# Performance work log

Measured on AMD Instinct MI355X. Metric: run time of the kernel, lower is better.

Reference implementation:

```python
import jax, jax.numpy as jnp
import numpy as np

H, KVH, D, THETA = 32, 8, 128, 10000.0

def _rotate_half(x):
    x1, x2 = x[..., : D // 2], x[..., D // 2 :]
    return jnp.concatenate((-x2, x1), axis=-1)

def _rope_tables(seq_len, dtype):
    inv_freq = 1.0 / (THETA ** (jnp.arange(0, D, 2, dtype=jnp.float32) / D))
    t = jnp.arange(seq_len, dtype=jnp.float32)
    freqs = jnp.outer(t, inv_freq)                # [S, D/2]
    emb = jnp.concatenate((freqs, freqs), axis=-1)  # [S, D]
    return jnp.cos(emb).astype(dtype), jnp.sin(emb).astype(dtype)

def setup_inputs() -> dict:
    key = jax.random.key(0)
    ks = jax.random.split(key, 6)
    B, S, HID = 1, 2048, H * D
    hidden_states = jax.random.normal(ks[0], (B, S, HID), jnp.float32)
    # additive causal mask (bsz, 1, q_len, kv_seq_len)
    causal = jnp.tril(jnp.ones((S, S), dtype=bool))
    attention_mask = jnp.where(causal, 0.0, jnp.finfo(jnp.float32).min)[None, None].astype(jnp.float32)
    position_ids = jnp.arange(S, dtype=jnp.int32)[None, :]
    sc = 0.02
    Wq = jax.random.normal(ks[1], (H * D, HID), jnp.float32) * sc
    Wk = jax.random.normal(ks[2], (KVH * D, HID), jnp.float32) * sc
    Wv = jax.random.normal(ks[3], (KVH * D, HID), jnp.float32) * sc
    Wo = jax.random.normal(ks[4], (HID, H * D), jnp.float32) * sc
    return dict(hidden_states=hidden_states, attention_mask=attention_mask,
                position_ids=position_ids, Wq=Wq, Wk=Wk, Wv=Wv, Wo=Wo)

def reference(hidden_states, attention_mask, position_ids, Wq, Wk, Wv, Wo):
    B, S, HID = hidden_states.shape
    n_rep = H // KVH
    # projections -> [B, h, S, D]
    q = (hidden_states @ Wq.T).reshape(B, S, H, D).transpose(0, 2, 1, 3)
    k = (hidden_states @ Wk.T).reshape(B, S, KVH, D).transpose(0, 2, 1, 3)
    v = (hidden_states @ Wv.T).reshape(B, S, KVH, D).transpose(0, 2, 1, 3)
    # RoPE (cos/sin gathered by position_ids, broadcast over heads)
    cos_t, sin_t = _rope_tables(S, hidden_states.dtype)
    cos = cos_t[position_ids][:, None]            # [B, 1, S, D]
    sin = sin_t[position_ids][:, None]
    q = q * cos + _rotate_half(q) * sin
    k = k * cos + _rotate_half(k) * sin
    # GQA: repeat_kv == repeat_interleave over head dim
    k = jnp.repeat(k, n_rep, axis=1)
    v = jnp.repeat(v, n_rep, axis=1)
    scores = jnp.einsum('bhqd,bhkd->bhqk', q, k) / jnp.sqrt(jnp.float32(D)).astype(q.dtype)
    scores = scores + attention_mask
    probs = jax.nn.softmax(scores.astype(jnp.float32), axis=-1).astype(q.dtype)
    attn = jnp.einsum('bhqk,bhkd->bhqd', probs, v)  # [B, H, S, D]
    attn = attn.transpose(0, 2, 1, 3).reshape(B, S, H * D)
    return attn @ Wo.T
```

## Files before the change

kernel.cpp:

```cpp
#include <hip/hip_runtime.h>
#include <hip/hip_bf16.h>

typedef __bf16 bf16;
typedef __attribute__((ext_vector_type(8))) __bf16 bf16x8;
typedef __attribute__((ext_vector_type(2))) __bf16 bf16x2;
typedef __attribute__((ext_vector_type(4))) float f32x4;

#define GLL16(g, l)                                                        \
  __builtin_amdgcn_global_load_lds(                                        \
      (const __attribute__((address_space(1))) unsigned int*)(g),          \
      (__attribute__((address_space(3))) unsigned int*)(l), 16, 0, 0)

__global__ void cvt_f32_bf16(const float* __restrict__ in,
                             bf16* __restrict__ out, long n) {
  long i = ((long)blockIdx.x * blockDim.x + threadIdx.x) * 8;
  if (i >= n) return;
  f32x4 a = *reinterpret_cast<const f32x4*>(in + i);
  f32x4 b = *reinterpret_cast<const f32x4*>(in + i + 4);
  bf16x8 o;
  o[0] = (bf16)a[0]; o[1] = (bf16)a[1]; o[2] = (bf16)a[2]; o[3] = (bf16)a[3];
  o[4] = (bf16)b[0]; o[5] = (bf16)b[1]; o[6] = (bf16)b[2]; o[7] = (bf16)b[3];
  *reinterpret_cast<bf16x8*>(out + i) = o;
}

template <typename CT>
__device__ __forceinline__ void gemm_body(const bf16* __restrict__ A,
                                          const float* __restrict__ B,
                                          CT* __restrict__ C,
                                          int bm, int bn, int N, int K) {
  __shared__ __align__(16) bf16 As[2][4096];
  __shared__ __align__(16) bf16 Bs[2][4096];
  const int t = threadIdx.x;
  const int lane = t & 63;
  const int w = t >> 6;
  const int wr = w >> 2, wc = w & 3;
  const int fr = lane & 15, fg = lane >> 4;

  const int sr = t >> 2;
  const int sc = (t & 3) * 8;
  const bf16* gA = A + (long)(bm + sr) * K + sc;
  const float* gB = B + (long)(bn + sr) * K + sc;

  f32x4 acc[4][2];
#pragma unroll
  for (int m = 0; m < 4; m++)
#pragma unroll
    for (int n = 0; n < 2; n++) acc[m][n] = (f32x4){0.f, 0.f, 0.f, 0.f};

  auto stageB = [&](int buf, int k0) {
    f32x4 b0 = *reinterpret_cast<const f32x4*>(gB + k0);
    f32x4 b1 = *reinterpret_cast<const f32x4*>(gB + k0 + 4);
    bf16x8 bb;
    bb[0] = (bf16)b0[0]; bb[1] = (bf16)b0[1];
    bb[2] = (bf16)b0[2]; bb[3] = (bf16)b0[3];
    bb[4] = (bf16)b1[0]; bb[5] = (bf16)b1[1];
    bb[6] = (bf16)b1[2]; bb[7] = (bf16)b1[3];
    *reinterpret_cast<bf16x8*>(&Bs[buf][t * 8]) = bb;
  };

  {
    GLL16(gA, &As[0][t * 8]);
    stageB(0, 0);
  }
  int cur = 0;
  for (int k0 = 0; k0 < K; k0 += 32) {
    __syncthreads();
    if (k0 + 32 < K) {
      GLL16(gA + k0 + 32, &As[cur ^ 1][t * 8]);
      stageB(cur ^ 1, k0 + 32);
    }
    bf16x8 af[4], bfr[2];
#pragma unroll
    for (int m = 0; m < 4; m++)
      af[m] = *reinterpret_cast<const bf16x8*>(
          &As[cur][(wr * 64 + m * 16 + fr) * 32 + fg * 8]);
#pragma unroll
    for (int n = 0; n < 2; n++)
      bfr[n] = *reinterpret_cast<const bf16x8*>(
          &Bs[cur][(wc * 32 + n * 16 + fr) * 32 + fg * 8]);
#pragma unroll
    for (int m = 0; m < 4; m++)
#pragma unroll
      for (int n = 0; n < 2; n++)
        acc[m][n] =
            __builtin_amdgcn_mfma_f32_16x16x32_bf16(af[m], bfr[n], acc[m][n], 0, 0, 0);
    cur ^= 1;
  }
#pragma unroll
  for (int m = 0; m < 4; m++) {
#pragma unroll
    for (int n = 0; n < 2; n++) {
      const int row0 = bm + wr * 64 + m * 16 + fg * 4;
      const int col = bn + wc * 32 + n * 16 + fr;
#pragma unroll
      for (int j = 0; j < 4; j++)
        C[(long)(row0 + j) * N + col] = (CT)acc[m][n][j];
    }
  }
}

template <typename CT>
__global__ __launch_bounds__(512)
void gemm_bt(const bf16* __restrict__ A, const float* __restrict__ B,
             CT* __restrict__ C, int M, int N, int K) {
  gemm_body<CT>(A, B, C, blockIdx.y * 128, blockIdx.x * 128, N, K);
}

__global__ __launch_bounds__(512)
void gemm_qkv(const bf16* __restrict__ A, const float* __restrict__ Wq,
              const float* __restrict__ Wk, const float* __restrict__ Wv,
              bf16* __restrict__ qo, bf16* __restrict__ ko,
              bf16* __restrict__ vo) {
  const int nb = blockIdx.x;
  const float* B; bf16* C; int bn, N;
  if (nb < 32)      { B = Wq; C = qo; bn = nb * 128;        N = 4096; }
  else if (nb < 40) { B = Wk; C = ko; bn = (nb - 32) * 128; N = 1024; }
  else              { B = Wv; C = vo; bn = (nb - 40) * 128; N = 1024; }
  gemm_body<bf16>(A, B, C, blockIdx.y * 128, bn, N, 4096);
}

__global__ void rope_kernel(bf16* __restrict__ q, bf16* __restrict__ k,
                            const int* __restrict__ pos_ids) {
  int idx = blockIdx.x * blockDim.x + threadIdx.x;
  int s = idx / 2560;
  int rem = idx % 2560;
  int hh = rem >> 6;
  int dp = rem & 63;
  float p = (float)pos_ids[s];
  float freq = p * exp2f(-(float)dp * 0.20762050593046025f);
  float cs, sn;
  sincosf(freq, &sn, &cs);
  bf16* base = (hh < 32) ? (q + (long)s * 4096 + hh * 128)
                         : (k + (long)s * 1024 + (hh - 32) * 128);
  float x1 = (float)base[dp], x2 = (float)base[dp + 64];
  base[dp] = (bf16)(x1 * cs - x2 * sn);
  base[dp + 64] = (bf16)(x2 * cs + x1 * sn);
}

__global__ __launch_bounds__(256, 2)
void attn_fwd(const bf16* __restrict__ qg, const bf16* __restrict__ kg,
              const bf16* __restrict__ vg, bf16* __restrict__ og) {
  const int h = blockIdx.y;
  const int kvh = h >> 2;
  __shared__ __align__(16) bf16 Ks[64 * 128];
  __shared__ __align__(16) bf16 Vt[128 * 64];
  __shared__ __align__(16) bf16 Pm[4][16 * 64];
  const int t = threadIdx.x, lane = t & 63, w = t >> 6;
  const int fr = lane & 15, fg = lane >> 4;
  const float scale = 0.08838834764831845f;

  const int krow = t >> 2, kcol = (t & 3) * 32;
  const int vr = (t & 31) * 2, vd0 = (t >> 5) * 8;
  const bf16* gK = kg + kvh * 128;
  const bf16* gV = vg + kvh * 128;

#pragma unroll 1
  for (int half = 0; half < 2; half++) {
    const int qt = half == 0 ? (int)blockIdx.x : 31 - (int)blockIdx.x;
    const int q0 = qt * 64;
    const int wqmax = q0 + w * 16 + 15;
    const int qrow = q0 + w * 16 + fr;
    const int nt = qt + 1;

    bf16x8 aq[4];
#pragma unroll
    for (int c = 0; c < 4; c++)
      aq[c] = *reinterpret_cast<const bf16x8*>(
          &qg[(long)qrow * 4096 + h * 128 + c * 32 + fg * 8]);

    f32x4 oacc[8];
#pragma unroll
    for (int n = 0; n < 8; n++) oacc[n] = (f32x4){0.f, 0.f, 0.f, 0.f};
    float mrow[4], lrow[4];
#pragma unroll
    for (int j = 0; j < 4; j++) { mrow[j] = -INFINITY; lrow[j] = 0.f; }

    bf16x8 kst[4], vst[4];
    {
      const bf16* gk = gK + (long)krow * 1024 + kcol;
#pragma unroll
      for (int i = 0; i < 4; i++)
        kst[i] = *reinterpret_cast<const bf16x8*>(gk + 8 * i);
      const bf16* gv = gV + (long)vr * 1024 + vd0;
      vst[0] = *reinterpret_cast<const bf16x8*>(gv);
      vst[1] = *reinterpret_cast<const bf16x8*>(gv + 64);
      vst[2] = *reinterpret_cast<const bf16x8*>(gv + 1024);
      vst[3] = *reinterpret_cast<const bf16x8*>(gv + 1024 + 64);
    }

    for (int tt = 0; tt < nt; ++tt) {
      const int kv0 = tt * 64;
#pragma unroll
      for (int i = 0; i < 4; i++)
        *reinterpret_cast<bf16x8*>(
            &Ks[krow * 128 + ((kcol + 8 * i) ^ ((krow & 7) << 3))]) = kst[i];
#pragma unroll
      for (int hv = 0; hv < 2; hv++)
#pragma unroll
        for (int j = 0; j < 8; j++) {
          const int d = hv * 64 + vd0 + j;
          bf16x2 pr;
          pr[0] = vst[hv][j];
          pr[1] = vst[2 + hv][j];
          *reinterpret_cast<bf16x2*>(&Vt[d * 64 + (vr ^ ((d & 7) << 3))]) = pr;
        }
      __syncthreads();

      if (tt + 1 < nt) {
        const long off = (long)(kv0 + 64) * 1024;
        const bf16* gk = gK + off + (long)krow * 1024 + kcol;
#pragma unroll
        for (int i = 0; i < 4; i++)
          kst[i] = *reinterpret_cast<const bf16x8*>(gk + 8 * i);
        const bf16* gv = gV + off + (long)vr * 1024 + vd0;
        vst[0] = *reinterpret_cast<const bf16x8*>(gv);
        vst[1] = *reinterpret_cast<const bf16x8*>(gv + 64);
        vst[2] = *reinterpret_cast<const bf16x8*>(gv + 1024);
        vst[3] = *reinterpret_cast<const bf16x8*>(gv + 1024 + 64);
      }

      f32x4 sacc[4];
#pragma unroll
      for (int c = 0; c < 4; c++) sacc[c] = (f32x4){0.f, 0.f, 0.f, 0.f};
#pragma unroll
      for (int c = 0; c < 4; c++) {
        if (kv0 + c * 16 <= wqmax) {
#pragma unroll
          for (int kc = 0; kc < 4; kc++) {
            const int row = c * 16 + fr;
            bf16x8 bk = *reinterpret_cast<const bf16x8*>(
                &Ks[row * 128 + ((kc * 32 + fg * 8) ^ ((row & 7) << 3))]);
            sacc[c] =
                __builtin_amdgcn_mfma_f32_16x16x32_bf16(aq[kc], bk, sacc[c], 0, 0, 0);
          }
        }
      }

#pragma unroll
      for (int j = 0; j < 4; j++) {
        const int qrel = q0 + w * 16 + fg * 4 + j - kv0;
        float s0 = (fr <= qrel) ? sacc[0][j] * scale : -INFINITY;
        float s1 = (16 + fr <= qrel) ? sacc[1][j] * scale : -INFINITY;
        float s2 = (32 + fr <= qrel) ? sacc[2][j] * scale : -INFINITY;
        float s3 = (48 + fr <= qrel) ? sacc[3][j] * scale : -INFINITY;
        float rmax = fmaxf(fmaxf(s0, s1), fmaxf(s2, s3));
#pragma unroll
        for (int off = 1; off < 16; off <<= 1)
          rmax = fmaxf(rmax, __shfl_xor(rmax, off, 64));
        const float mnew = fmaxf(mrow[j], rmax);
        const float alpha = __expf(mrow[j] - mnew);
        mrow[j] = mnew;
        const float p0 = __expf(s0 - mnew);
        const float p1 = __expf(s1 - mnew);
        const float p2 = __expf(s2 - mnew);
        const float p3 = __expf(s3 - mnew);
        float rsum = (p0 + p1) + (p2 + p3);
#pragma unroll
        for (int off = 1; off < 16; off <<= 1) rsum += __shfl_xor(rsum, off, 64);
        lrow[j] = lrow[j] * alpha + rsum;
#pragma unroll
        for (int n = 0; n < 8; n++) oacc[n][j] *= alpha;
        const int prow = fg * 4 + j;
        const int psw = (prow & 7) << 3;
        Pm[w][prow * 64 + (fr ^ psw)] = (bf16)p0;
        Pm[w][prow * 64 + ((16 + fr) ^ psw)] = (bf16)p1;
        Pm[w][prow * 64 + ((32 + fr) ^ psw)] = (bf16)p2;
        Pm[w][prow * 64 + ((48 + fr) ^ psw)] = (bf16)p3;
      }

      const int asw = (fr & 7) << 3;
      bf16x8 ap0 = *reinterpret_cast<const bf16x8*>(
          &Pm[w][fr * 64 + ((fg * 8) ^ asw)]);
      bf16x8 ap1 = *reinterpret_cast<const bf16x8*>(
          &Pm[w][fr * 64 + ((32 + fg * 8) ^ asw)]);
#pragma unroll
      for (int n = 0; n < 8; n++) {
        const int dr = n * 16 + fr;
        const int dsw = (dr & 7) << 3;
        bf16x8 bv0 = *reinterpret_cast<const bf16x8*>(
            &Vt[dr * 64 + ((fg * 8) ^ dsw)]);
        bf16x8 bv1 = *reinterpret_cast<const bf16x8*>(
            &Vt[dr * 64 + ((32 + fg * 8) ^ dsw)]);
        oacc[n] = __builtin_amdgcn_mfma_f32_16x16x32_bf16(ap0, bv0, oacc[n], 0, 0, 0);
        oacc[n] = __builtin_amdgcn_mfma_f32_16x16x32_bf16(ap1, bv1, oacc[n], 0, 0, 0);
      }
      __syncthreads();
    }

#pragma unroll
    for (int n = 0; n < 8; n++) {
#pragma unroll
      for (int j = 0; j < 4; j++) {
        const int row = q0 + w * 16 + fg * 4 + j;
        const int col = h * 128 + n * 16 + fr;
        og[(long)row * 4096 + col] = (bf16)(oacc[n][j] / lrow[j]);
      }
    }
  }
}

extern "C" void kernel_launch(void* const* d_in, const int* in_sizes, int n_in,
                              void* d_out, int out_size, void* d_ws,
                              size_t ws_size, hipStream_t stream) {
  const float* hs = (const float*)d_in[0];
  const int* pos = (const int*)d_in[2];
  const float* Wq = (const float*)d_in[3];
  const float* Wk = (const float*)d_in[4];
  const float* Wv = (const float*)d_in[5];
  const float* Wo = (const float*)d_in[6];

  char* ws = (char*)d_ws;
  bf16* h_bf  = (bf16*)(ws);
  bf16* q_bf  = (bf16*)(ws + 16777216L);
  bf16* k_bf  = (bf16*)(ws + 33554432L);
  bf16* v_bf  = (bf16*)(ws + 37748736L);
  bf16* at_bf = h_bf;

  cvt_f32_bf16<<<dim3(4096), 256, 0, stream>>>(hs, h_bf, 8388608L);

  gemm_qkv<<<dim3(48, 16), 512, 0, stream>>>(h_bf, Wq, Wk, Wv,
                                             q_bf, k_bf, v_bf);

  rope_kernel<<<dim3(20480), 256, 0, stream>>>(q_bf, k_bf, pos);

  attn_fwd<<<dim3(16, 32), 256, 0, stream>>>(q_bf, k_bf, v_bf, at_bf);

  gemm_bt<float><<<dim3(32, 16), 512, 0, stream>>>(at_bf, Wo, (float*)d_out,
                                                   2048, 4096, 4096);
}
```

Measured before the change: 419.8 us.

## Fuse RoPE into QKV projection GEMM epilogue via LDS partner exchange

Removes the separate rope kernel and applies rotary embedding in the QKV GEMM epilogue for Q and K tiles. The 128-column tile covers one head, so each wave swaps accumulators with its partner wave (wc^2) through shared memory to get the rotate-half element, computes sincos per element, and writes the rotated bf16. This saves a launch plus one read-modify-write pass over Q and K. In exchange it adds two syncs and redundant sincos calls in the epilogue, and inlines its own GEMM main loop instead of calling gemm_body.

```diff
diff --git a/kernel.cpp b/kernel.cpp
--- a/kernel.cpp
+++ b/kernel.cpp
@@ -109,32 +109,129 @@
 __global__ __launch_bounds__(512)
 void gemm_qkv(const bf16* __restrict__ A, const float* __restrict__ Wq,
               const float* __restrict__ Wk, const float* __restrict__ Wv,
-              bf16* __restrict__ qo, bf16* __restrict__ ko,
-              bf16* __restrict__ vo) {
+              const int* __restrict__ pos, bf16* __restrict__ qo,
+              bf16* __restrict__ ko, bf16* __restrict__ vo) {
+  __shared__ __align__(16) bf16 smem[4][4096];
+  bf16(*As)[4096] = &smem[0];
+  bf16(*Bs)[4096] = &smem[2];
+
   const int nb = blockIdx.x;
   const float* B; bf16* C; int bn, N;
   if (nb < 32)      { B = Wq; C = qo; bn = nb * 128;        N = 4096; }
   else if (nb < 40) { B = Wk; C = ko; bn = (nb - 32) * 128; N = 1024; }
   else              { B = Wv; C = vo; bn = (nb - 40) * 128; N = 1024; }
-  gemm_body<bf16>(A, B, C, blockIdx.y * 128, bn, N, 4096);
-}
-
-__global__ void rope_kernel(bf16* __restrict__ q, bf16* __restrict__ k,
-                            const int* __restrict__ pos_ids) {
-  int idx = blockIdx.x * blockDim.x + threadIdx.x;
-  int s = idx / 2560;
-  int rem = idx % 2560;
-  int hh = rem >> 6;
-  int dp = rem & 63;
-  float p = (float)pos_ids[s];
-  float freq = p * exp2f(-(float)dp * 0.20762050593046025f);
-  float cs, sn;
-  sincosf(freq, &sn, &cs);
-  bf16* base = (hh < 32) ? (q + (long)s * 4096 + hh * 128)
-                         : (k + (long)s * 1024 + (hh - 32) * 128);
-  float x1 = (float)base[dp], x2 = (float)base[dp + 64];
-  base[dp] = (bf16)(x1 * cs - x2 * sn);
-  base[dp + 64] = (bf16)(x2 * cs + x1 * sn);
+  const int bm = blockIdx.y * 128;
+  const int K = 4096;
+
+  const int t = threadIdx.x;
+  const int lane = t & 63;
+  const int w = t >> 6;
+  const int wr = w >> 2, wc = w & 3;
+  const int fr = lane & 15, fg = lane >> 4;
+
+  const int sr = t >> 2;
+  const int sc = (t & 3) * 8;
+  const bf16* gA = A + (long)(bm + sr) * K + sc;
+  const float* gB = B + (long)(bn + sr) * K + sc;
+
+  f32x4 acc[4][2];
+#pragma unroll
+  for (int m = 0; m < 4; m++)
+#pragma unroll
+    for (int n = 0; n < 2; n++) acc[m][n] = (f32x4){0.f, 0.f, 0.f, 0.f};
+
+  auto stageB = [&](int buf, int k0) {
+    f32x4 b0 = *reinterpret_cast<const f32x4*>(gB + k0);
+    f32x4 b1 = *reinterpret_cast<const f32x4*>(gB + k0 + 4);
+    bf16x8 bb;
+    bb[0] = (bf16)b0[0]; bb[1] = (bf16)b0[1];
+    bb[2] = (bf16)b0[2]; bb[3] = (bf16)b0[3];
+    bb[4] = (bf16)b1[0]; bb[5] = (bf16)b1[1];
+    bb[6] = (bf16)b1[2]; bb[7] = (bf16)b1[3];
+    *reinterpret_cast<bf16x8*>(&Bs[buf][t * 8]) = bb;
+  };
+
+  {
+    GLL16(gA, &As[0][t * 8]);
+    stageB(0, 0);
+  }
+  int cur = 0;
+  for (int k0 = 0; k0 < K; k0 += 32) {
+    __syncthreads();
+    if (k0 + 32 < K) {
+      GLL16(gA + k0 + 32, &As[cur ^ 1][t * 8]);
+      stageB(cur ^ 1, k0 + 32);
+    }
+    bf16x8 af[4], bfr[2];
+#pragma unroll
+    for (int m = 0; m < 4; m++)
+      af[m] = *reinterpret_cast<const bf16x8*>(
+          &As[cur][(wr * 64 + m * 16 + fr) * 32 + fg * 8]);
+#pragma unroll
+    for (int n = 0; n < 2; n++)
+      bfr[n] = *reinterpret_cast<const bf16x8*>(
+          &Bs[cur][(wc * 32 + n * 16 + fr) * 32 + fg * 8]);
+#pragma unroll
+    for (int m = 0; m < 4; m++)
+#pragma unroll
+      for (int n = 0; n < 2; n++)
+        acc[m][n] =
+            __builtin_amdgcn_mfma_f32_16x16x32_bf16(af[m], bfr[n], acc[m][n], 0, 0, 0);
+    cur ^= 1;
+  }
+
+  if (nb >= 40) {
+#pragma unroll
+    for (int m = 0; m < 4; m++)
+#pragma unroll
+      for (int n = 0; n < 2; n++) {
+        const int row0 = bm + wr * 64 + m * 16 + fg * 4;
+        const int col = bn + wc * 32 + n * 16 + fr;
+#pragma unroll
+        for (int j = 0; j < 4; j++)
+          C[(long)(row0 + j) * N + col] = (bf16)acc[m][n][j];
+      }
+    return;
+  }
+
+  float* stage = reinterpret_cast<float*>(smem);
+  for (int wrg = 0; wrg < 2; wrg++) {
+    __syncthreads();
+    if (wr == wrg) {
+      float* st = &stage[(wc * 64 + lane) * 32];
+#pragma unroll
+      for (int m = 0; m < 4; m++)
+#pragma unroll
+        for (int n = 0; n < 2; n++)
+#pragma unroll
+          for (int j = 0; j < 4; j++) st[m * 8 + n * 4 + j] = acc[m][n][j];
+    }
+    __syncthreads();
+    if (wr == wrg) {
+      const float* pt = &stage[((wc ^ 2) * 64 + lane) * 32];
+#pragma unroll
+      for (int n = 0; n < 2; n++) {
+        const int col = wc * 32 + n * 16 + fr;
+        const int dp = col & 63;
+        const bool hi = col >= 64;
+        const float invf = exp2f(-(float)dp * 0.20762050593046025f);
+#pragma unroll
+        for (int m = 0; m < 4; m++) {
+#pragma unroll
+          for (int j = 0; j < 4; j++) {
+            const int row = bm + wr * 64 + m * 16 + fg * 4 + j;
+            const float fq = (float)pos[row] * invf;
+            float cs, sn;
+            sincosf(fq, &sn, &cs);
+            const float x = acc[m][n][j];
+            const float xp = pt[m * 8 + n * 4 + j];
+            const float o = hi ? x * cs + xp * sn : x * cs - xp * sn;
+            C[(long)row * N + bn + col] = (bf16)o;
+          }
+        }
+      }
+    }
+  }
 }
 
 __global__ __launch_bounds__(256, 2)
@@ -318,10 +415,8 @@
 
   cvt_f32_bf16<<<dim3(4096), 256, 0, stream>>>(hs, h_bf, 8388608L);
 
-  gemm_qkv<<<dim3(48, 16), 512, 0, stream>>>(h_bf, Wq, Wk, Wv,
+  gemm_qkv<<<dim3(48, 16), 512, 0, stream>>>(h_bf, Wq, Wk, Wv, pos,
                                              q_bf, k_bf, v_bf);
-
-  rope_kernel<<<dim3(20480), 256, 0, stream>>>(q_bf, k_bf, pos);
 
   attn_fwd<<<dim3(16, 32), 256, 0, stream>>>(q_bf, k_bf, v_bf, at_bf);
 
```

New measurement: 458.9 us. 9.3% more time.

## Register-prefetch GEMM tiles two steps ahead with XOR-swizzled LDS layout

Applied to the files above, without the earlier changes.

Replaces the direct global-to-LDS load for A with register loads, and prefetches both the A and B tiles for step k+2 into registers while step k computes. The registers are written into the other LDS buffer at the start of the next iteration. The LDS tile layout changes to a k-chunk-major arrangement with an XOR swizzle on the row index, to reduce bank conflicts on the 16-byte fragment reads. The sync moves to the end of each iteration. This hides global latency better but raises register pressure and gives up the asynchronous LDS DMA path for A.

```diff
diff --git a/kernel.cpp b/kernel.cpp
--- a/kernel.cpp
+++ b/kernel.cpp
@@ -5,11 +5,6 @@
 typedef __attribute__((ext_vector_type(8))) __bf16 bf16x8;
 typedef __attribute__((ext_vector_type(2))) __bf16 bf16x2;
 typedef __attribute__((ext_vector_type(4))) float f32x4;
-
-#define GLL16(g, l)                                                        \
-  __builtin_amdgcn_global_load_lds(                                        \
-      (const __attribute__((address_space(1))) unsigned int*)(g),          \
-      (__attribute__((address_space(3))) unsigned int*)(l), 16, 0, 0)
 
 __global__ void cvt_f32_bf16(const float* __restrict__ in,
                              bf16* __restrict__ out, long n) {
@@ -37,9 +32,10 @@
   const int fr = lane & 15, fg = lane >> 4;
 
   const int sr = t >> 2;
-  const int sc = (t & 3) * 8;
-  const bf16* gA = A + (long)(bm + sr) * K + sc;
-  const float* gB = B + (long)(bn + sr) * K + sc;
+  const int sch = t & 3;
+  const int wsl = sch * 1024 + (sr ^ (sch << 2)) * 8;
+  const bf16* gA = A + (long)(bm + sr) * K + sch * 8;
+  const float* gB = B + (long)(bn + sr) * K + sch * 8;
 
   f32x4 acc[4][2];
 #pragma unroll
@@ -47,43 +43,53 @@
 #pragma unroll
     for (int n = 0; n < 2; n++) acc[m][n] = (f32x4){0.f, 0.f, 0.f, 0.f};
 
-  auto stageB = [&](int buf, int k0) {
-    f32x4 b0 = *reinterpret_cast<const f32x4*>(gB + k0);
-    f32x4 b1 = *reinterpret_cast<const f32x4*>(gB + k0 + 4);
+  bf16x8 ra;
+  f32x4 rb0, rb1;
+  auto loads = [&](int k0) {
+    ra = *reinterpret_cast<const bf16x8*>(gA + k0);
+    rb0 = *reinterpret_cast<const f32x4*>(gB + k0);
+    rb1 = *reinterpret_cast<const f32x4*>(gB + k0 + 4);
+  };
+  auto writes = [&](int buf) {
+    *reinterpret_cast<bf16x8*>(&As[buf][wsl]) = ra;
     bf16x8 bb;
-    bb[0] = (bf16)b0[0]; bb[1] = (bf16)b0[1];
-    bb[2] = (bf16)b0[2]; bb[3] = (bf16)b0[3];
-    bb[4] = (bf16)b1[0]; bb[5] = (bf16)b1[1];
-    bb[6] = (bf16)b1[2]; bb[7] = (bf16)b1[3];
-    *reinterpret_cast<bf16x8*>(&Bs[buf][t * 8]) = bb;
+    bb[0] = (bf16)rb0[0]; bb[1] = (bf16)rb0[1];
+    bb[2] = (bf16)rb0[2]; bb[3] = (bf16)rb0[3];
+    bb[4] = (bf16)rb1[0]; bb[5] = (bf16)rb1[1];
+    bb[6] = (bf16)rb1[2]; bb[7] = (bf16)rb1[3];
+    *reinterpret_cast<bf16x8*>(&Bs[buf][wsl]) = bb;
   };
 
-  {
-    GLL16(gA, &As[0][t * 8]);
-    stageB(0, 0);
-  }
+  loads(0);
+  writes(0);
+  loads(32);
+  __syncthreads();
   int cur = 0;
   for (int k0 = 0; k0 < K; k0 += 32) {
-    __syncthreads();
     if (k0 + 32 < K) {
-      GLL16(gA + k0 + 32, &As[cur ^ 1][t * 8]);
-      stageB(cur ^ 1, k0 + 32);
+      writes(cur ^ 1);
+      if (k0 + 64 < K) loads(k0 + 64);
     }
     bf16x8 af[4], bfr[2];
 #pragma unroll
-    for (int m = 0; m < 4; m++)
+    for (int m = 0; m < 4; m++) {
+      const int r = wr * 64 + m * 16 + fr;
       af[m] = *reinterpret_cast<const bf16x8*>(
-          &As[cur][(wr * 64 + m * 16 + fr) * 32 + fg * 8]);
-#pragma unroll
-    for (int n = 0; n < 2; n++)
+          &As[cur][fg * 1024 + (r ^ (fg << 2)) * 8]);
+    }
+#pragma unroll
+    for (int n = 0; n < 2; n++) {
+      const int r = wc * 32 + n * 16 + fr;
       bfr[n] = *reinterpret_cast<const bf16x8*>(
-          &Bs[cur][(wc * 32 + n * 16 + fr) * 32 + fg * 8]);
+          &Bs[cur][fg * 1024 + (r ^ (fg << 2)) * 8]);
+    }
 #pragma unroll
     for (int m = 0; m < 4; m++)
 #pragma unroll
       for (int n = 0; n < 2; n++)
         acc[m][n] =
             __builtin_amdgcn_mfma_f32_16x16x32_bf16(af[m], bfr[n], acc[m][n], 0, 0, 0);
+    __syncthreads();
     cur ^= 1;
   }
 #pragma unroll
```

New measurement: 359.5 us. 1.17x faster.
